# Optimization experiments

Measured on AMD Instinct MI355X. Metric: run time of the kernel, lower is better.

Reference implementation:

```python
import jax, jax.numpy as jnp
import numpy as np

N = 100000   # nodes
E = 300000   # edges
D = 256      # emb_dim
L = 5        # num_layers
SELF_LOOP_BOND_TYPE = 4
BN_EPS = 1e-5


def setup_inputs() -> dict:
    key = jax.random.key(0)
    ks = jax.random.split(key, 12)
    s = 0.05
    x = jax.random.randint(ks[0], (N, 2), 0, 3)
    edge_index = jax.random.randint(ks[1], (2, E), 0, N)
    edge_attr = jax.random.randint(ks[2], (E, 2), 0, 3)
    x_emb1 = jax.random.normal(ks[3], (120, D), dtype=jnp.float32) * s
    x_emb2 = jax.random.normal(ks[4], (3, D), dtype=jnp.float32) * s
    edge_emb1 = jax.random.normal(ks[5], (L, 6, D), dtype=jnp.float32) * s
    edge_emb2 = jax.random.normal(ks[6], (L, 3, D), dtype=jnp.float32) * s
    W1 = jax.random.normal(ks[7], (L, D, 2 * D), dtype=jnp.float32) * (1.0 / np.sqrt(D))
    b1 = jnp.zeros((L, 2 * D), dtype=jnp.float32)
    W2 = jax.random.normal(ks[8], (L, 2 * D, D), dtype=jnp.float32) * (1.0 / np.sqrt(2 * D))
    b2 = jnp.zeros((L, D), dtype=jnp.float32)
    bn_gamma = jnp.ones((L - 1, D), dtype=jnp.float32)
    bn_beta = jnp.zeros((L - 1, D), dtype=jnp.float32)
    return dict(x=x, edge_index=edge_index, edge_attr=edge_attr,
                x_emb1=x_emb1, x_emb2=x_emb2,
                edge_emb1=edge_emb1, edge_emb2=edge_emb2,
                W1=W1, b1=b1, W2=W2, b2=b2,
                bn_gamma=bn_gamma, bn_beta=bn_beta)


def reference(x, edge_index, edge_attr, x_emb1, x_emb2, edge_emb1, edge_emb2,
              W1, b1, W2, b2, bn_gamma, bn_beta):
    n = x.shape[0]
    loop = jnp.arange(n)
    # add_self_loops: append (i, i) for every node
    src = jnp.concatenate([edge_index[0], loop])  # [E+N]
    dst = jnp.concatenate([edge_index[1], loop])  # [E+N]
    # self-loop edge_attr = (bond_type=4, direction=0)
    self_attr = jnp.concatenate([
        jnp.full((n, 1), SELF_LOOP_BOND_TYPE, dtype=edge_attr.dtype),
        jnp.zeros((n, 1), dtype=edge_attr.dtype)], axis=1)
    ea = jnp.concatenate([edge_attr, self_attr], axis=0)  # [E+N, 2]

    out = x_emb1[x[:, 0]] + x_emb2[x[:, 1]]  # [N, D]
    for l in range(L):
        e_emb = edge_emb1[l][ea[:, 0]] + edge_emb2[l][ea[:, 1]]  # [E+N, D]
        msg = out[src] + e_emb                                   # gather + message
        agg = jax.ops.segment_sum(msg, dst, num_segments=n)      # scatter-add
        h = jax.nn.relu(agg @ W1[l] + b1[l]) @ W2[l] + b2[l]     # GIN MLP
        if l < L - 1:
            mean = h.mean(axis=0)
            var = h.var(axis=0)  # biased var, matches torch BN training
            h = (h - mean) * jax.lax.rsqrt(var + BN_EPS) * bn_gamma[l] + bn_beta[l]
            h = jax.nn.relu(h)
        out = h
    return out
```

## Files before the change

### kernel.cpp

```cpp
#include <hip/hip_runtime.h>

typedef unsigned short u16;
typedef unsigned int u32;
typedef unsigned char u8;

#define DD 256
#define PLCAP 1536

typedef short  s16x8 __attribute__((ext_vector_type(8)));
typedef short  s16x4 __attribute__((ext_vector_type(4)));
typedef float  f32x4 __attribute__((ext_vector_type(4)));
typedef float  f32x16 __attribute__((ext_vector_type(16)));

__device__ __forceinline__ float b2f(u16 u){
  union { u32 i; float f; } c; c.i = ((u32)u) << 16; return c.f;
}
__device__ __forceinline__ u16 f2b(float f){
  union { float f; u32 i; } c; c.f = f;
  u32 b = c.i + 0x7FFFu + ((c.i >> 16) & 1u);
  return (u16)(b >> 16);
}

__global__ void NodeEncoder_72971494359603_kernel(){}

__global__ void probe_dtype(const u32* w, u32* flag){
  if (threadIdx.x == 0 && blockIdx.x == 0){
    int cnt = 0;
    for (int i = 0; i < 256; i++){
      u32 low = w[i] & 0xFFFFu;
      u32 e = (low >> 7) & 0xFFu;
      if (e >= 0x60u && e <= 0x7Eu) cnt++;
    }
    *flag = (cnt >= 192) ? 1u : 0u;
  }
}

struct CvtArgs {
  const void* src[10];
  u16* dst[10];
  int n[10];
};
__global__ void cvt_batch(CvtArgs a, const u32* __restrict__ flag){
  int i = blockIdx.x * 256 + threadIdx.x;
  u32 f = *flag;
#pragma unroll
  for (int s = 0; s < 10; s++){
    if (i < a.n[s]){
      if (f) a.dst[s][i] = ((const u16*)a.src[s])[i];
      else   a.dst[s][i] = f2b(((const float*)a.src[s])[i]);
      return;
    }
    i -= a.n[s];
  }
}

__global__ void zero_int(int* p, int n){
  int i = blockIdx.x * 256 + threadIdx.x;
  if (i < n) p[i] = 0;
}

__global__ void build_table(const u16* ee1, const u16* ee2, u16* TBL){
  int b = blockIdx.x;
  int l = b / 18, c = b % 18, a = c / 3, bb = c % 3;
  int j = threadIdx.x;
  TBL[b * DD + j] = f2b(b2f(ee1[(l * 6 + a) * DD + j]) + b2f(ee2[(l * 3 + bb) * DD + j]));
}

__global__ void build_emb9(const u16* xe1, const u16* xe2, u16* EMB9){
  int c = blockIdx.x;
  int j = threadIdx.x;
  EMB9[c * DD + j] = f2b(b2f(xe1[(c / 3) * DD + j]) + b2f(xe2[(c % 3) * DD + j]));
}

__global__ void gen_codes(const int* x, u8* codes, int N){
  int n = blockIdx.x * 256 + threadIdx.x;
  if (n < N){
    int x0 = x[2 * n], x1 = x[2 * n + 1];
    x0 = x0 < 0 ? 0 : (x0 > 2 ? 2 : x0);
    x1 = x1 < 0 ? 0 : (x1 > 2 ? 2 : x1);
    codes[n] = (u8)(x0 * 3 + x1);
  }
}

__global__ void hist_kernel(const int* dst, int* counts, int E){
  int e = blockIdx.x * 256 + threadIdx.x;
  if (e < E) atomicAdd(&counts[dst[e]], 1);
}

__global__ void scan_sums(const int* counts, int* bsum, int N){
  __shared__ int red[256];
  int tid = threadIdx.x;
  int base = blockIdx.x * 1024;
  int s = 0;
  for (int i = tid; i < 1024; i += 256){
    int g = base + i;
    if (g < N) s += counts[g];
  }
  red[tid] = s;
  __syncthreads();
  for (int off = 128; off > 0; off >>= 1){
    if (tid < off) red[tid] += red[tid + off];
    __syncthreads();
  }
  if (tid == 0) bsum[blockIdx.x] = red[0];
}

__global__ void scan_top(int* bsum, int nb){
  if (threadIdx.x == 0 && blockIdx.x == 0){
    int acc = 0;
    for (int i = 0; i < nb; i++){ int t = bsum[i]; bsum[i] = acc; acc += t; }
  }
}

__global__ void scan_block(const int* counts, const int* bsum,
                           int* offsets, int* cursor, int N){
  __shared__ int tsum[256];
  int b = blockIdx.x;
  int tid = threadIdx.x;
  int base = b * 1024;
  int v0, v1, v2, v3;
  int g = base + tid * 4;
  v0 = (g + 0 < N) ? counts[g + 0] : 0;
  v1 = (g + 1 < N) ? counts[g + 1] : 0;
  v2 = (g + 2 < N) ? counts[g + 2] : 0;
  v3 = (g + 3 < N) ? counts[g + 3] : 0;
  tsum[tid] = v0 + v1 + v2 + v3;
  __syncthreads();
  for (int off = 1; off < 256; off <<= 1){
    int t = (tid >= off) ? tsum[tid - off] : 0;
    __syncthreads();
    tsum[tid] += t;
    __syncthreads();
  }
  int excl = (tid == 0 ? 0 : tsum[tid - 1]) + bsum[b];
  if (g + 0 < N){ offsets[g + 0] = excl; cursor[g + 0] = excl; } excl += v0;
  if (g + 1 < N){ offsets[g + 1] = excl; cursor[g + 1] = excl; } excl += v1;
  if (g + 2 < N){ offsets[g + 2] = excl; cursor[g + 2] = excl; } excl += v2;
  if (g + 3 < N){ offsets[g + 3] = excl; cursor[g + 3] = excl; }
}

__global__ void fill_csr(const int* ei, const int* ea, const int* x,
                         int* cursor, int* payload, int E){
  int e = blockIdx.x * 256 + threadIdx.x;
  if (e < E){
    int d = ei[E + e];
    int src = ei[e];
    int pos = atomicAdd(&cursor[d], 1);
    int a = ea[2 * e], bb = ea[2 * e + 1];
    int x0 = x[2 * src], x1 = x[2 * src + 1];
    x0 = x0 < 0 ? 0 : (x0 > 2 ? 2 : x0);
    x1 = x1 < 0 ? 0 : (x1 > 2 ? 2 : x1);
    payload[pos] = src | ((a * 3 + bb) << 17) | ((x0 * 3 + x1) << 22);
  }
}

__global__ void pack_B(const u16* __restrict__ W0, u16* __restrict__ Wp0, int K, int Nc){
  const u16* W = W0 + (size_t)blockIdx.y * K * Nc;
  u16* Wp = Wp0 + (size_t)blockIdx.y * K * Nc;
  int idx = blockIdx.x * 256 + threadIdx.x;
  int lane = idx & 63;
  int t = idx >> 6;
  int nk = K >> 4;
  int kstep = t % nk, cblk = t / nk;
  if (cblk >= (Nc >> 5)) return;
  int col = cblk * 32 + (lane & 31);
  int krow = kstep * 16 + (lane >> 5) * 8;
  u16* dst = Wp + (size_t)idx * 8;
#pragma unroll
  for (int e = 0; e < 8; e++)
    dst[e] = W[(size_t)(krow + e) * Nc + col];
}

__global__ __launch_bounds__(512, 4)
void layer_fused(const u16* __restrict__ feat, const u16* __restrict__ TBL,
                 const int* __restrict__ offsets, const int* __restrict__ counts,
                 const int* __restrict__ payload,
                 const u16* __restrict__ Wp1, const u16* __restrict__ bias1,
                 const u16* __restrict__ Wp2, const u16* __restrict__ bias2,
                 u16* __restrict__ H, float* __restrict__ partial, int npart, int M,
                 const float* __restrict__ sums, const u16* __restrict__ gamma,
                 const u16* __restrict__ beta, float invN, int apply_bn,
                 const u16* __restrict__ EMB9, const u8* __restrict__ codes, int use_emb,
                 void* __restrict__ dout, const u32* __restrict__ dflag){
  __shared__ __align__(16) u16 As[64 * 256];
  __shared__ __align__(16) u16 Ms[2][64 * 128];
  u16* T  = (u16*)Ms;
  u16* EM = (u16*)((char*)Ms + 9216);
  int* PL = (int*)((char*)Ms + 13824);
  int tid = threadIdx.x, lane = tid & 63, wave = tid >> 6;
  int wr = wave >> 2, wc = wave & 3;
  int row0 = blockIdx.x * 64;
  int l31 = lane & 31, lhi = lane >> 5;

  {
    u32* Tw = (u32*)T;
    const u32* Gw = (const u32*)TBL;
    for (int i = tid; i < 18 * DD / 2; i += 512) Tw[i] = Gw[i];
    if (use_emb){
      u32* Ew = (u32*)EM;
      const u32* Sw = (const u32*)EMB9;
      for (int i = tid; i < 9 * DD / 2; i += 512) Ew[i] = Sw[i];
    }
  }
  int nlast = row0 + 63; if (nlast > M - 1) nlast = M - 1;
  int e_start = offsets[row0];
  int e_total = offsets[nlast] + counts[nlast] - e_start;
  for (int i = tid; i < e_total && i < PLCAP; i += 512) PL[i] = payload[e_start + i];
  __syncthreads();

  if (use_emb){
    int c4 = lane * 4;
    s16x4 tb = *(const s16x4*)(T + 12 * DD + c4);
    for (int u = 0; u < 8; u++){
      int r = wave * 8 + u;
      int n = row0 + r; if (n > M - 1) n = M - 1;
      int cd = codes[n];
      s16x4 ev = *(const s16x4*)(EM + cd * DD + c4);
      float a0 = b2f((u16)ev[0]) + b2f((u16)tb[0]);
      float a1 = b2f((u16)ev[1]) + b2f((u16)tb[1]);
      float a2 = b2f((u16)ev[2]) + b2f((u16)tb[2]);
      float a3 = b2f((u16)ev[3]) + b2f((u16)tb[3]);
      int e0 = offsets[n], eend = e0 + counts[n];
      for (int e = e0; e < eend; e++){
        int idx = e - e_start;
        int pl = (idx < PLCAP) ? PL[idx] : payload[e];
        s16x4 rv = *(const s16x4*)(EM + ((pl >> 22) & 15) * DD + c4);
        s16x4 tv = *(const s16x4*)(T + ((pl >> 17) & 31) * DD + c4);
        a0 += b2f((u16)rv[0]) + b2f((u16)tv[0]);
        a1 += b2f((u16)rv[1]) + b2f((u16)tv[1]);
        a2 += b2f((u16)rv[2]) + b2f((u16)tv[2]);
        a3 += b2f((u16)rv[3]) + b2f((u16)tv[3]);
      }
      s16x4 o;
      o[0] = (short)f2b(a0); o[1] = (short)f2b(a1);
      o[2] = (short)f2b(a2); o[3] = (short)f2b(a3);
      int byteo = r * 512 + (((lane >> 1) ^ (r & 31)) << 4) + ((lane & 1) << 3);
      *(s16x4*)((char*)As + byteo) = o;
    }
  } else {
    int c4 = lane * 4;
    float sc[4], sh[4];
    if (apply_bn){
#pragma unroll
      for (int e = 0; e < 4; e++){
        int j = c4 + e;
        float mean = sums[j] * invN;
        float var = sums[DD + j] * invN - mean * mean;
        if (var < 0.f) var = 0.f;
        float scl = rsqrtf(var + 1e-5f) * b2f(gamma[j]);
        sc[e] = scl; sh[e] = b2f(beta[j]) - mean * scl;
      }
    } else {
#pragma unroll
      for (int e = 0; e < 4; e++){ sc[e] = 1.f; sh[e] = 0.f; }
    }
    int rbase = wave * 8;
    int offs[8], cnts[8]; s16x4 sv[8];
#pragma unroll
    for (int u = 0; u < 8; u++){
      int n = row0 + rbase + u; if (n > M - 1) n = M - 1;
      offs[u] = offsets[n]; cnts[u] = counts[n];
      sv[u] = *(const s16x4*)(feat + (size_t)n * DD + c4);
    }
    s16x4 tb = *(const s16x4*)(T + 12 * DD + c4);
#pragma unroll
    for (int up = 0; up < 2; up++){
      float a[4][4];
#pragma unroll
      for (int h = 0; h < 4; h++){
        s16x4 svv = sv[up * 4 + h];
#pragma unroll
        for (int j = 0; j < 4; j++){
          float v = b2f((u16)svv[j]) * sc[j] + sh[j];
          if (apply_bn) v = fmaxf(v, 0.f);
          a[h][j] = v + b2f((u16)tb[j]);
        }
      }
      int eo[4], cn[4], ii[4];
#pragma unroll
      for (int h = 0; h < 4; h++){
        eo[h] = offs[up * 4 + h]; cn[h] = cnts[up * 4 + h]; ii[h] = 0;
      }
      while (ii[0] < cn[0] || ii[1] < cn[1] || ii[2] < cn[2] || ii[3] < cn[3]){
        int bb[4]; int pls[4][4]; s16x4 rv[4][4];
#pragma unroll
        for (int h = 0; h < 4; h++){
          int t = cn[h] - ii[h];
          bb[h] = t > 4 ? 4 : (t < 0 ? 0 : t);
        }
#pragma unroll
        for (int h = 0; h < 4; h++)
#pragma unroll
          for (int i = 0; i < 4; i++)
            if (i < bb[h]){
              int idx = eo[h] + ii[h] + i - e_start;
              pls[h][i] = (idx < PLCAP) ? PL[idx] : payload[eo[h] + ii[h] + i];
            }
#pragma unroll
        for (int h = 0; h < 4; h++)
#pragma unroll
          for (int i = 0; i < 4; i++)
            if (i < bb[h])
              rv[h][i] = *(const s16x4*)(feat + (size_t)(pls[h][i] & 0x1FFFF) * DD + c4);
#pragma unroll
        for (int h = 0; h < 4; h++)
#pragma unroll
          for (int i = 0; i < 4; i++)
            if (i < bb[h]){
              s16x4 tv = *(const s16x4*)(T + ((pls[h][i] >> 17) & 31) * DD + c4);
#pragma unroll
              for (int j = 0; j < 4; j++){
                float w = b2f((u16)rv[h][i][j]) * sc[j] + sh[j];
                if (apply_bn) w = fmaxf(w, 0.f);
                a[h][j] += w + b2f((u16)tv[j]);
              }
            }
#pragma unroll
        for (int h = 0; h < 4; h++) ii[h] += bb[h];
      }
#pragma unroll
      for (int h = 0; h < 4; h++){
        int r = rbase + up * 4 + h;
        s16x4 o;
        o[0] = (short)f2b(a[h][0]); o[1] = (short)f2b(a[h][1]);
        o[2] = (short)f2b(a[h][2]); o[3] = (short)f2b(a[h][3]);
        int byteo = r * 512 + (((lane >> 1) ^ (r & 31)) << 4) + ((lane & 1) << 3);
        *(s16x4*)((char*)As + byteo) = o;
      }
    }
  }
  __syncthreads();

  f32x16 acc2[2];
#pragma unroll
  for (int n = 0; n < 2; n++)
#pragma unroll
    for (int i = 0; i < 16; i++) acc2[n][i] = 0.f;
  f32x16 acc1;

  auto G1 = [&](int cc){
    f32x16 a1;
#pragma unroll
    for (int i = 0; i < 16; i++) a1[i] = 0.f;
    int arow = wr * 32 + l31;
    int cb = cc * 4 + wc;
#pragma unroll
    for (int ks = 0; ks < 16; ks++){
      int slot = (ks * 2 + lhi) ^ (arow & 31);
      s16x8 af = *(const s16x8*)((const char*)As + arow * 512 + (slot << 4));
      s16x8 bf = *(const s16x8*)(Wp1 + (((size_t)cb * 16 + ks) * 64 + lane) * 8);
      a1 = __builtin_amdgcn_mfma_f32_32x32x16_bf16(af, bf, a1, 0, 0, 0);
    }
    acc1 = a1;
  };
  auto WMS = [&](int cc, int buf){
    char* ms = (char*)Ms[buf];
    int col = wc * 32 + l31;
    float bv = b2f(bias1[cc * 128 + col]);
#pragma unroll
    for (int reg = 0; reg < 16; reg++){
      int mrow = wr * 32 + (reg & 3) + 8 * (reg >> 2) + 4 * lhi;
      float v = fmaxf(acc1[reg] + bv, 0.f);
      int slot = (col >> 3) ^ (mrow & 15);
      *(u16*)(ms + mrow * 256 + (slot << 4) + (col & 7) * 2) = f2b(v);
    }
  };

  G1(0);
  WMS(0, 0);
  __syncthreads();

#pragma unroll
  for (int c = 0; c < 4; c++){
    const char* ms = (const char*)Ms[c & 1];
    int mrow = wr * 32 + l31;
#pragma unroll
    for (int ks = 0; ks < 8; ks++){
      int slot = (ks * 2 + lhi) ^ (mrow & 15);
      s16x8 mf = *(const s16x8*)(ms + mrow * 256 + (slot << 4));
#pragma unroll
      for (int n = 0; n < 2; n++){
        int cb2 = wc * 2 + n;
        s16x8 wf = *(const s16x8*)(Wp2 + (((size_t)cb2 * 32 + c * 8 + ks) * 64 + lane) * 8);
        acc2[n] = __builtin_amdgcn_mfma_f32_32x32x16_bf16(mf, wf, acc2[n], 0, 0, 0);
      }
    }
    if (c < 3){
      G1(c + 1);
      WMS(c + 1, (c + 1) & 1);
      __syncthreads();
    }
  }

#pragma unroll
  for (int n = 0; n < 2; n++){
    int col = wc * 64 + n * 32 + l31;
    float bv = b2f(bias2[col]);
#pragma unroll
    for (int reg = 0; reg < 16; reg++){
      int row = wr * 32 + (reg & 3) + 8 * (reg >> 2) + 4 * lhi;
      int slot = (col >> 3) ^ (row & 31);
      *(u16*)((char*)As + row * 512 + (slot << 4) + (col & 7) * 2) = f2b(acc2[n][reg] + bv);
    }
  }
  __syncthreads();

  float s[8], q[8];
#pragma unroll
  for (int e = 0; e < 8; e++){ s[e] = 0.f; q[e] = 0.f; }
  int sl = tid & 31;
  u32 df = dout ? *dflag : 0u;
#pragma unroll
  for (int p = 0; p < 4; p++){
    int r = p * 16 + (tid >> 5);
    s16x8 v = *(const s16x8*)((const char*)As + r * 512 + ((sl ^ (r & 31)) << 4));
    int gr = row0 + r;
    if (gr < M){
      if (dout){
        if (df){
          *(s16x8*)((u16*)dout + (size_t)gr * DD + sl * 8) = v;
        } else {
          f32x4 o0, o1;
#pragma unroll
          for (int e = 0; e < 4; e++){ o0[e] = b2f((u16)v[e]); o1[e] = b2f((u16)v[4 + e]); }
          *(f32x4*)((float*)dout + (size_t)gr * DD + sl * 8) = o0;
          *(f32x4*)((float*)dout + (size_t)gr * DD + sl * 8 + 4) = o1;
        }
      } else {
        *(s16x8*)(H + (size_t)gr * DD + sl * 8) = v;
      }
      if (partial){
#pragma unroll
        for (int e = 0; e < 8; e++){
          float f = b2f((u16)v[e]);
          s[e] += f; q[e] += f * f;
        }
      }
    }
  }
  if (partial){
#pragma unroll
    for (int e = 0; e < 8; e++){
      s[e] += __shfl_xor(s[e], 32);
      q[e] += __shfl_xor(q[e], 32);
    }
    __syncthreads();
    float* redS = (float*)Ms;
    float* redQ = redS + 8 * 256;
    if (lane < 32){
#pragma unroll
      for (int e = 0; e < 8; e++){
        redS[wave * 256 + sl * 8 + e] = s[e];
        redQ[wave * 256 + sl * 8 + e] = q[e];
      }
    }
    __syncthreads();
    if (tid < 256){
      float a = 0.f, b = 0.f;
#pragma unroll
      for (int w = 0; w < 8; w++){ a += redS[w * 256 + tid]; b += redQ[w * 256 + tid]; }
      partial[(size_t)blockIdx.x * DD + tid] = a;
      partial[(size_t)(npart + blockIdx.x) * DD + tid] = b;
    }
  }
}

__global__ void bn_reduce(const float* __restrict__ partial, float* __restrict__ sums,
                          int npart){
  int b = blockIdx.x, which = b >> 3, jg = b & 7;
  int t = threadIdx.x;
  int j = jg * 32 + (t >> 3);
  int li = t & 7;
  float s = 0.f;
  for (int i = li; i < npart; i += 8)
    s += partial[(size_t)(which * npart + i) * DD + j];
  s += __shfl_xor(s, 1); s += __shfl_xor(s, 2); s += __shfl_xor(s, 4);
  if (li == 0) sums[which * DD + j] = s;
}

extern "C" void kernel_launch(void* const* d_in, const int* in_sizes, int n_in,
                              void* d_out, int out_size, void* d_ws, size_t ws_size,
                              hipStream_t stream){
  (void)n_in; (void)out_size; (void)ws_size;
  const int* x    = (const int*)d_in[0];
  const int* ei   = (const int*)d_in[1];
  const int* ea   = (const int*)d_in[2];
  const void* xe1 = d_in[3];
  const void* xe2 = d_in[4];
  const void* ee1 = d_in[5];
  const void* ee2 = d_in[6];
  const void* W1  = d_in[7];
  const void* b1  = d_in[8];
  const void* W2  = d_in[9];
  const void* b2  = d_in[10];
  const void* gam = d_in[11];
  const void* bet = d_in[12];

  int N = in_sizes[0] / 2;
  int E = in_sizes[1] / 2;
  int NB = (N + 1023) / 1024;
  const int L = 5;
  int nblk = (N + 63) / 64;
  int npart = nblk;

  char* base = (char*)d_ws;
  size_t off = 0;
  u32* flag    = (u32*)(base + off);   off += 256;
  u16* TBL     = (u16*)(base + off);   off += ((size_t)L * 18 * DD * 2 + 255) & ~(size_t)255;
  u16* EMB9    = (u16*)(base + off);   off += ((size_t)9 * DD * 2 + 255) & ~(size_t)255;
  u8* codes    = (u8*)(base + off);    off += ((size_t)N + 255) & ~(size_t)255;
  int* counts  = (int*)(base + off);   off += ((size_t)N * 4 + 255) & ~(size_t)255;
  int* offsets = (int*)(base + off);   off += ((size_t)N * 4 + 255) & ~(size_t)255;
  int* cursor  = (int*)(base + off);   off += ((size_t)N * 4 + 255) & ~(size_t)255;
  int* bsum    = (int*)(base + off);   off += ((size_t)NB * 4 + 255) & ~(size_t)255;
  int* payload = (int*)(base + off);   off += ((size_t)E * 4 + 255) & ~(size_t)255;
  float* part  = (float*)(base + off); off += ((size_t)2 * npart * DD * 4 + 255) & ~(size_t)255;
  float* sums  = (float*)(base + off); off += ((size_t)2 * DD * 4 + 255) & ~(size_t)255;
  u16* wx1  = (u16*)(base + off); off += ((size_t)120 * DD * 2 + 255) & ~(size_t)255;
  u16* wx2  = (u16*)(base + off); off += ((size_t)3 * DD * 2 + 255) & ~(size_t)255;
  u16* wee1 = (u16*)(base + off); off += ((size_t)L * 6 * DD * 2 + 255) & ~(size_t)255;
  u16* wee2 = (u16*)(base + off); off += ((size_t)L * 3 * DD * 2 + 255) & ~(size_t)255;
  u16* wW1  = (u16*)(base + off); off += ((size_t)L * DD * 2 * DD * 2 + 255) & ~(size_t)255;
  u16* wb1  = (u16*)(base + off); off += ((size_t)L * 2 * DD * 2 + 255) & ~(size_t)255;
  u16* wW2  = (u16*)(base + off); off += ((size_t)L * 2 * DD * DD * 2 + 255) & ~(size_t)255;
  u16* wb2  = (u16*)(base + off); off += ((size_t)L * DD * 2 + 255) & ~(size_t)255;
  u16* wgam = (u16*)(base + off); off += ((size_t)(L - 1) * DD * 2 + 255) & ~(size_t)255;
  u16* wbet = (u16*)(base + off); off += ((size_t)(L - 1) * DD * 2 + 255) & ~(size_t)255;
  u16* Wp1  = (u16*)(base + off); off += ((size_t)L * DD * 2 * DD * 2 + 255) & ~(size_t)255;
  u16* Wp2  = (u16*)(base + off); off += ((size_t)L * 2 * DD * DD * 2 + 255) & ~(size_t)255;
  u16* featA = (u16*)(base + off); off += ((size_t)N * DD * 2 + 255) & ~(size_t)255;
  u16* featB = (u16*)(base + off); off += ((size_t)N * DD * 2 + 255) & ~(size_t)255;

  probe_dtype<<<1, 64, 0, stream>>>((const u32*)xe1, flag);
  {
    CvtArgs ca;
    const void* srcs[10] = { xe1, xe2, ee1, ee2, W1, b1, W2, b2, gam, bet };
    u16* dsts[10] = { wx1, wx2, wee1, wee2, wW1, wb1, wW2, wb2, wgam, wbet };
    int ns[10] = { 120 * DD, 3 * DD, L * 6 * DD, L * 3 * DD, L * DD * 2 * DD,
                   L * 2 * DD, L * 2 * DD * DD, L * DD, (L - 1) * DD, (L - 1) * DD };
    int total = 0;
    for (int i = 0; i < 10; i++){ ca.src[i] = srcs[i]; ca.dst[i] = dsts[i]; ca.n[i] = ns[i]; total += ns[i]; }
    cvt_batch<<<(total + 255) / 256, 256, 0, stream>>>(ca, flag);
  }

  build_table<<<90, 256, 0, stream>>>(wee1, wee2, TBL);
  build_emb9<<<9, 256, 0, stream>>>(wx1, wx2, EMB9);
  gen_codes<<<(N + 255) / 256, 256, 0, stream>>>(x, codes, N);
  pack_B<<<dim3(64, L), 256, 0, stream>>>(wW1, Wp1, DD, 2 * DD);
  pack_B<<<dim3(64, L), 256, 0, stream>>>(wW2, Wp2, 2 * DD, DD);
  zero_int<<<(N + 255) / 256, 256, 0, stream>>>(counts, N);
  hist_kernel<<<(E + 255) / 256, 256, 0, stream>>>(ei + E, counts, E);
  scan_sums<<<NB, 256, 0, stream>>>(counts, bsum, N);
  scan_top<<<1, 64, 0, stream>>>(bsum, NB);
  scan_block<<<NB, 256, 0, stream>>>(counts, bsum, offsets, cursor, N);
  fill_csr<<<(E + 255) / 256, 256, 0, stream>>>(ei, ea, x, cursor, payload, E);

  float invN = 1.0f / (float)N;
  u16* fin = featA;
  u16* fout = featB;

  for (int l = 0; l < L; l++){
    int last = (l == L - 1);
    layer_fused<<<nblk, 512, 0, stream>>>(
        fin, TBL + (size_t)l * 18 * DD, offsets, counts, payload,
        Wp1 + (size_t)l * DD * 2 * DD, wb1 + (size_t)l * 2 * DD,
        Wp2 + (size_t)l * 2 * DD * DD, wb2 + (size_t)l * DD,
        fout, (l < L - 1) ? part : (float*)nullptr, npart, N,
        sums, wgam + (size_t)(l > 0 ? l - 1 : 0) * DD,
        wbet + (size_t)(l > 0 ? l - 1 : 0) * DD, invN, l > 0 ? 1 : 0,
        EMB9, codes, l == 0 ? 1 : 0,
        last ? d_out : (void*)nullptr, flag);

    if (l < L - 1){
      bn_reduce<<<16, 256, 0, stream>>>(part, sums, npart);
    }
    u16* t = fin; fin = fout; fout = t;
  }
}
```

Before: 1.361 ms.

## Stage neighbor gathers into LDS via global_load_lds over flattened edge stream

The neighbor aggregation no longer walks four destination rows in lockstep, where the loop runs as long as the longest row. Each wave now processes one contiguous edge range covering all 8 of its rows, in batches of 8 edges. Each source feature row is copied straight into a per-wave LDS staging area with global_load_lds, then read back from LDS and accumulated into the right destination row, selected with per-edge compare chains. The aim is to balance work across uneven degrees and cut VGPR pressure from register-held gathered rows. In exchange it adds a full vmcnt(0) wait per batch, which limits how many loads are in flight, plus extra branching to pick the destination row.

```diff
diff --git a/kernel.cpp b/kernel.cpp
--- a/kernel.cpp
+++ b/kernel.cpp
@@ -263,70 +263,74 @@
       sv[u] = *(const s16x4*)(feat + (size_t)n * DD + c4);
     }
     s16x4 tb = *(const s16x4*)(T + 12 * DD + c4);
-#pragma unroll
-    for (int up = 0; up < 2; up++){
-      float a[4][4];
-#pragma unroll
-      for (int h = 0; h < 4; h++){
-        s16x4 svv = sv[up * 4 + h];
-#pragma unroll
-        for (int j = 0; j < 4; j++){
-          float v = b2f((u16)svv[j]) * sc[j] + sh[j];
-          if (apply_bn) v = fmaxf(v, 0.f);
-          a[h][j] = v + b2f((u16)tb[j]);
+
+    float a[8][4];
+#pragma unroll
+    for (int h = 0; h < 8; h++){
+      s16x4 svv = sv[h];
+#pragma unroll
+      for (int j = 0; j < 4; j++){
+        float v = b2f((u16)svv[j]) * sc[j] + sh[j];
+        if (apply_bn) v = fmaxf(v, 0.f);
+        a[h][j] = v + b2f((u16)tb[j]);
+      }
+    }
+
+    char* stg = (char*)As + wave * 4096;
+    int e_lo = offs[0];
+    int e_hi = offs[7] + cnts[7];
+    int h = 0;
+    for (int b0 = e_lo; b0 < e_hi; b0 += 8){
+      int nb = e_hi - b0; if (nb > 8) nb = 8;
+      int pls[8];
+#pragma unroll
+      for (int i = 0; i < 8; i++){
+        if (i < nb){
+          int e = b0 + i;
+          int idx = e - e_start;
+          int pl = (idx < PLCAP) ? PL[idx] : payload[e];
+          pls[i] = pl;
+          const u32* gsrc = (const u32*)(feat + (size_t)(pl & 0x1FFFF) * DD);
+          __builtin_amdgcn_global_load_lds(gsrc + lane, (u32*)(stg + i * 512), 4, 0, 0);
+          __builtin_amdgcn_global_load_lds(gsrc + 64 + lane, (u32*)(stg + i * 512 + 256), 4, 0, 0);
         }
       }
-      int eo[4], cn[4], ii[4];
-#pragma unroll
-      for (int h = 0; h < 4; h++){
-        eo[h] = offs[up * 4 + h]; cn[h] = cnts[up * 4 + h]; ii[h] = 0;
-      }
-      while (ii[0] < cn[0] || ii[1] < cn[1] || ii[2] < cn[2] || ii[3] < cn[3]){
-        int bb[4]; int pls[4][4]; s16x4 rv[4][4];
-#pragma unroll
-        for (int h = 0; h < 4; h++){
-          int t = cn[h] - ii[h];
-          bb[h] = t > 4 ? 4 : (t < 0 ? 0 : t);
+      asm volatile("s_waitcnt vmcnt(0)" ::: "memory");
+#pragma unroll
+      for (int i = 0; i < 8; i++){
+        if (i < nb){
+          int e = b0 + i;
+#pragma unroll
+          for (int hh = 0; hh < 7; hh++)
+            if (h == hh && e >= offs[hh + 1]) h++;
+          int pl = pls[i];
+          s16x4 rv = *(const s16x4*)(stg + i * 512 + lane * 8);
+          s16x4 tv = *(const s16x4*)(T + ((pl >> 17) & 31) * DD + c4);
+          float w[4];
+#pragma unroll
+          for (int j = 0; j < 4; j++){
+            float ww = b2f((u16)rv[j]) * sc[j] + sh[j];
+            if (apply_bn) ww = fmaxf(ww, 0.f);
+            w[j] = ww + b2f((u16)tv[j]);
+          }
+#pragma unroll
+          for (int hh = 0; hh < 8; hh++)
+            if (h == hh){
+#pragma unroll
+              for (int j = 0; j < 4; j++) a[hh][j] += w[j];
+            }
         }
-#pragma unroll
-        for (int h = 0; h < 4; h++)
-#pragma unroll
-          for (int i = 0; i < 4; i++)
-            if (i < bb[h]){
-              int idx = eo[h] + ii[h] + i - e_start;
-              pls[h][i] = (idx < PLCAP) ? PL[idx] : payload[eo[h] + ii[h] + i];
-            }
-#pragma unroll
-        for (int h = 0; h < 4; h++)
-#pragma unroll
-          for (int i = 0; i < 4; i++)
-            if (i < bb[h])
-              rv[h][i] = *(const s16x4*)(feat + (size_t)(pls[h][i] & 0x1FFFF) * DD + c4);
-#pragma unroll
-        for (int h = 0; h < 4; h++)
-#pragma unroll
-          for (int i = 0; i < 4; i++)
-            if (i < bb[h]){
-              s16x4 tv = *(const s16x4*)(T + ((pls[h][i] >> 17) & 31) * DD + c4);
-#pragma unroll
-              for (int j = 0; j < 4; j++){
-                float w = b2f((u16)rv[h][i][j]) * sc[j] + sh[j];
-                if (apply_bn) w = fmaxf(w, 0.f);
-                a[h][j] += w + b2f((u16)tv[j]);
-              }
-            }
-#pragma unroll
-        for (int h = 0; h < 4; h++) ii[h] += bb[h];
-      }
-#pragma unroll
-      for (int h = 0; h < 4; h++){
-        int r = rbase + up * 4 + h;
-        s16x4 o;
-        o[0] = (short)f2b(a[h][0]); o[1] = (short)f2b(a[h][1]);
-        o[2] = (short)f2b(a[h][2]); o[3] = (short)f2b(a[h][3]);
-        int byteo = r * 512 + (((lane >> 1) ^ (r & 31)) << 4) + ((lane & 1) << 3);
-        *(s16x4*)((char*)As + byteo) = o;
-      }
+      }
+    }
+
+#pragma unroll
+    for (int hh = 0; hh < 8; hh++){
+      int r = rbase + hh;
+      s16x4 o;
+      o[0] = (short)f2b(a[hh][0]); o[1] = (short)f2b(a[hh][1]);
+      o[2] = (short)f2b(a[hh][2]); o[3] = (short)f2b(a[hh][3]);
+      int byteo = r * 512 + (((lane >> 1) ^ (r & 31)) << 4) + ((lane & 1) << 3);
+      *(s16x4*)((char*)As + byteo) = o;
     }
   }
   __syncthreads();
```

New measurement: 1.440 ms. +5.8%, slower.
